# Kernel tuning notes

Hardware: AMD Instinct MI355X
Metric: run time of the kernel (lower is better)

Reference implementation:

```python
import jax, jax.numpy as jnp
import numpy as np

EMBED_DIM = 1024
NUM_HEADS = 16
HEAD_DIM = EMBED_DIM // NUM_HEADS
SCALE = EMBED_DIM ** (-0.5)  # NOTE: module scales by embed_dim**-0.5, not head_dim**-0.5


def setup_inputs() -> dict:
    key = jax.random.key(0)
    ks = jax.random.split(key, 10)
    B, N = 2, 2048
    q = jax.random.normal(ks[0], (B, N, EMBED_DIM), dtype=jnp.float32)
    kv = jax.random.normal(ks[1], (B, N, EMBED_DIM), dtype=jnp.float32)
    mask = jax.random.randint(ks[2], (B, N), 0, 2, dtype=jnp.int64)
    s = 0.02
    Wq = jax.random.normal(ks[3], (EMBED_DIM, EMBED_DIM), dtype=jnp.float32) * s
    bq = jax.random.normal(ks[4], (EMBED_DIM,), dtype=jnp.float32) * s
    Wkv = jax.random.normal(ks[5], (EMBED_DIM, 2 * EMBED_DIM), dtype=jnp.float32) * s
    bkv = jax.random.normal(ks[6], (2 * EMBED_DIM,), dtype=jnp.float32) * s
    Wo = jax.random.normal(ks[7], (EMBED_DIM, EMBED_DIM), dtype=jnp.float32) * s
    bo = jax.random.normal(ks[8], (EMBED_DIM,), dtype=jnp.float32) * s
    return {"q": q, "kv": kv, "mask": mask, "Wq": Wq, "bq": bq,
            "Wkv": Wkv, "bkv": bkv, "Wo": Wo, "bo": bo}


def _softmax_plus_one(x):
    # softmax with +1 in the denominator; max clipped at 0, no grad through max
    m = jax.lax.stop_gradient(jnp.maximum(jnp.max(x, axis=-1, keepdims=True), 0.0))
    unnorm = jnp.exp(x - m)
    denom = jnp.sum(unnorm, axis=-1, keepdims=True) + jnp.exp(-m)
    return unnorm / denom


def _split_heads(x):
    b, n, _ = x.shape
    return x.reshape(b, n, NUM_HEADS, HEAD_DIM).transpose(0, 2, 1, 3)  # b h n d


def reference(q, kv, mask, Wq, bq, Wkv, bkv, Wo, bo):
    xq = q @ Wq + bq
    xkv = kv @ Wkv + bkv
    xk, xv = jnp.split(xkv, 2, axis=-1)
    xq, xk, xv = _split_heads(xq), _split_heads(xk), _split_heads(xv)
    logits = jnp.einsum('bhnd,bhmd->bhnm', xq * SCALE, xk)
    # prepare_mask: log of 0/1 mask broadcast over (head, query) dims
    logmask = jnp.log(mask.astype(logits.dtype))[:, None, None, :]
    logits = logits + logmask
    # attn_dropout = 0.0 -> no-op
    scores = _softmax_plus_one(logits)  # add_one_to_softmax=True
    attn = jnp.einsum('bhnm,bhmd->bhnd', scores, xv)
    b, h, n, d = attn.shape
    out = attn.transpose(0, 2, 1, 3).reshape(b, n, h * d)
    return out @ Wo + bo
```

## Files before the change

### kernel.cpp

```cpp
#include <hip/hip_runtime.h>
#include <hip/hip_bf16.h>

static constexpr int CB = 2, CN = 2048, CE = 1024, CH = 16, CD = 64;
static constexpr int CM = CB * CN;
#define SCALE_Q (1.4426950408889634f / 32.0f)

typedef __attribute__((ext_vector_type(8))) short short8;
typedef __attribute__((ext_vector_type(4))) float f32x4;
typedef __attribute__((ext_vector_type(16))) float f32x16;
typedef __attribute__((ext_vector_type(4))) float f4;
typedef __attribute__((ext_vector_type(4))) unsigned short u16x4;

#define MFMA16(a, b, c) __builtin_amdgcn_mfma_f32_16x16x32_bf16((a), (b), (c), 0, 0, 0)
#define MFMA32(a, b, c) __builtin_amdgcn_mfma_f32_32x32x16_bf16((a), (b), (c), 0, 0, 0)

static __device__ __forceinline__ unsigned short f2bf(float f) {
  union { __hip_bfloat16 h; unsigned short u; } cv;
  cv.h = __float2bfloat16(f);
  return cv.u;
}
static __device__ __forceinline__ unsigned int pk2bf(float lo, float hi) {
  return (unsigned int)f2bf(lo) | ((unsigned int)f2bf(hi) << 16);
}

typedef unsigned int u32;
static __device__ __forceinline__ void gload16(const void* g, void* l) {
  __builtin_amdgcn_global_load_lds(
      (const __attribute__((address_space(1))) u32*)g,
      (__attribute__((address_space(3))) u32*)l, 16, 0, 0);
}

__global__ __launch_bounds__(256) void prep(
    const float* __restrict__ Wq, const float* __restrict__ Wkv,
    const float* __restrict__ Wo, unsigned short* __restrict__ WqT,
    unsigned short* __restrict__ WkvT, unsigned short* __restrict__ WoT,
    const int* __restrict__ mask, int* __restrict__ cidx, int* __restrict__ cnt) {
  __shared__ float tile[32][33];
  __shared__ int tsum[256];
  const int bid = blockIdx.x;
  const int t = threadIdx.x;
  if (bid < 4096) {
    const float* in; unsigned short* out; int C, tb;
    if (bid < 1024)      { in = Wq;  out = WqT;  C = 1024; tb = bid; }
    else if (bid < 3072) { in = Wkv; out = WkvT; C = 2048; tb = bid - 1024; }
    else                 { in = Wo;  out = WoT;  C = 1024; tb = bid - 3072; }
    const int R = 1024;
    int tc = C >> 5;
    int bc = tb % tc, br = tb / tc;
    int c = t & 31, r0 = t >> 5;
#pragma unroll
    for (int i = 0; i < 4; ++i) {
      int r = r0 + i * 8;
      tile[r][c] = in[(size_t)(br * 32 + r) * C + bc * 32 + c];
    }
    __syncthreads();
#pragma unroll
    for (int i = 0; i < 4; ++i) {
      int r = r0 + i * 8;
      out[(size_t)(bc * 32 + r) * R + br * 32 + c] = f2bf(tile[c][r]);
    }
  } else {
    const int b = bid - 4096;
    int m[8], s = 0;
#pragma unroll
    for (int i = 0; i < 8; ++i) {
      m[i] = mask[b * CN + t * 8 + i] != 0;
      s += m[i];
    }
    tsum[t] = s;
    __syncthreads();
    if (t == 0) {
      int acc = 0;
      for (int i = 0; i < 256; ++i) { int v = tsum[i]; tsum[i] = acc; acc += v; }
      cnt[b] = acc;
    }
    __syncthreads();
    int pos = tsum[t];
#pragma unroll
    for (int i = 0; i < 8; ++i)
      if (m[i]) cidx[b * CN + pos++] = t * 8 + i;
  }
}

template <bool AF32, bool OUT_BF16, bool VSPLIT, bool GATHER>
static __device__ __forceinline__ void gemm_body(
    char* lds, int bm, int bn,
    const void* __restrict__ Ap, const unsigned short* __restrict__ Bt,
    const float* __restrict__ bias, void* __restrict__ C0,
    unsigned short* __restrict__ C1, int N, int K, float outscale,
    const int* __restrict__ cidx, const int* __restrict__ cnt) {
  constexpr int ASTR = AF32 ? 40 : 32;
  unsigned short* As = (unsigned short*)lds;
  unsigned short* Bs = (unsigned short*)(lds + 2 * 64 * ASTR * 2);
  const int m0 = bm << 6, n0 = bn << 7;

  if constexpr (GATHER) {
    const int bb = m0 >> 11;
    const int ru = min((cnt[bb] + 63) & ~63, CN);
    if ((m0 & 2047) >= ru) return;
  }

  const int t = threadIdx.x;
  const int lane = t & 63, w = t >> 6;
  const int wr = w >> 1, wc = w & 1;
  const int fr = lane & 15, fg = lane >> 4;

  const int ach = t & 3;
  size_t arow;
  {
    int gr = m0 + (t >> 2);
    if constexpr (GATHER) {
      int bb = gr >> 11, r = gr & 2047;
      int cb_ = cnt[bb];
      int cr = r < cb_ ? r : (cb_ > 0 ? cb_ - 1 : 0);
      gr = bb * CN + cidx[bb * CN + cr];
    }
    arow = (size_t)gr * K;
  }

  f32x4 acc[2][4];
#pragma unroll
  for (int i = 0; i < 2; ++i)
#pragma unroll
    for (int j = 0; j < 4; ++j) acc[i][j] = (f32x4){0.f, 0.f, 0.f, 0.f};

  f4 a0, a1;
  auto ALOAD = [&](int k0) {
    const float* src = (const float*)Ap + arow + k0 + ach * 8;
    a0 = *(const f4*)src;
    a1 = *(const f4*)(src + 4);
  };
  auto AWRITE = [&](int bi) {
    short8 av;
#pragma unroll
    for (int j = 0; j < 4; ++j) av[j] = (short)f2bf(a0[j]);
#pragma unroll
    for (int j = 0; j < 4; ++j) av[4 + j] = (short)f2bf(a1[j]);
    *(short8*)&As[bi * 64 * ASTR + (t >> 2) * ASTR + ach * 8] = av;
  };
  auto BSTAGE = [&](int bi, int k0) {
#pragma unroll
    for (int i = 0; i < 2; ++i) {
      int idx = t + i * 256, row = idx >> 2, ch = idx & 3;
      gload16(Bt + (size_t)(n0 + row) * K + k0 + ch * 8, &Bs[bi * 128 * 32 + idx * 8]);
    }
    if constexpr (!AF32)
      gload16((const unsigned short*)Ap + arow + k0 + ach * 8, &As[bi * 64 * 32 + t * 8]);
  };

  if constexpr (AF32) { ALOAD(0); AWRITE(0); }
  BSTAGE(0, 0);
  __syncthreads();

  const int nt = K >> 5;
  int buf = 0;
  for (int tt = 0; tt < nt; ++tt) {
    const bool np = tt < nt - 1;
    if (np) {
      if constexpr (AF32) ALOAD((tt + 1) << 5);
      BSTAGE(buf ^ 1, (tt + 1) << 5);
    }
    if (np) {
      if constexpr (AF32) asm volatile("s_waitcnt vmcnt(4)" ::: "memory");
      else                asm volatile("s_waitcnt vmcnt(3)" ::: "memory");
    } else {
      asm volatile("s_waitcnt vmcnt(0)" ::: "memory");
    }
    __builtin_amdgcn_s_barrier();
    __builtin_amdgcn_sched_barrier(0);

    short8 af[2], bfv[4];
#pragma unroll
    for (int mi = 0; mi < 2; ++mi)
      af[mi] = *(const short8*)&As[buf * 64 * ASTR + (wr * 32 + mi * 16 + fr) * ASTR + fg * 8];
#pragma unroll
    for (int ni = 0; ni < 4; ++ni)
      bfv[ni] = *(const short8*)&Bs[buf * 128 * 32 + (wc * 64 + ni * 16 + fr) * 32 + fg * 8];
#pragma unroll
    for (int mi = 0; mi < 2; ++mi)
#pragma unroll
      for (int ni = 0; ni < 4; ++ni) acc[mi][ni] = MFMA16(af[mi], bfv[ni], acc[mi][ni]);
    if (np) {
      if constexpr (AF32) AWRITE(buf ^ 1);
    }
    asm volatile("s_waitcnt lgkmcnt(0)" ::: "memory");
    __builtin_amdgcn_s_barrier();
    __builtin_amdgcn_sched_barrier(0);
    buf ^= 1;
  }

#pragma unroll
  for (int mi = 0; mi < 2; ++mi) {
    int row0 = m0 + wr * 32 + mi * 16 + fg * 4;
#pragma unroll
    for (int ni = 0; ni < 4; ++ni) {
      int col = n0 + wc * 64 + ni * 16 + fr;
      float bv = bias[col];
      if constexpr (VSPLIT) {
        if (col < CE) {
#pragma unroll
          for (int rr = 0; rr < 4; ++rr)
            ((unsigned short*)C0)[(size_t)(row0 + rr) * CE + col] =
                f2bf((acc[mi][ni][rr] + bv) * outscale);
        } else {
          u16x4 pk;
#pragma unroll
          for (int rr = 0; rr < 4; ++rr) pk[rr] = f2bf((acc[mi][ni][rr] + bv) * outscale);
          int b = row0 / CN, n = row0 % CN;
          *(u16x4*)&C1[((size_t)b * CE + (col - CE)) * CN + n] = pk;
        }
      } else if constexpr (OUT_BF16) {
#pragma unroll
        for (int rr = 0; rr < 4; ++rr)
          ((unsigned short*)C0)[(size_t)(row0 + rr) * N + col] =
              f2bf((acc[mi][ni][rr] + bv) * outscale);
      } else {
#pragma unroll
        for (int rr = 0; rr < 4; ++rr)
          ((float*)C0)[(size_t)(row0 + rr) * N + col] = (acc[mi][ni][rr] + bv) * outscale;
      }
    }
  }
}

__global__ __launch_bounds__(256) void gemm_qkv(
    const float* __restrict__ q, const unsigned short* __restrict__ WqT,
    const float* __restrict__ bq, unsigned short* __restrict__ xq,
    const float* __restrict__ kv, const unsigned short* __restrict__ WkvT,
    const float* __restrict__ bkv, unsigned short* __restrict__ xk,
    unsigned short* __restrict__ xvT,
    const int* __restrict__ cidx, const int* __restrict__ cnt) {
  __shared__ char lds[2 * 64 * 40 * 2 + 2 * 128 * 32 * 2];
  const int bid = blockIdx.x;
  if (bid < 512) {
    gemm_body<true, true, false, false>(lds, bid >> 3, bid & 7, q, WqT, bq,
                                        xq, nullptr, CE, CE, SCALE_Q,
                                        nullptr, nullptr);
  } else {
    const int b2 = bid - 512;
    gemm_body<true, true, true, true>(lds, b2 >> 4, b2 & 15, kv, WkvT, bkv,
                                      xk, xvT, 2 * CE, CE, 1.0f, cidx, cnt);
  }
}

__global__ __launch_bounds__(256) void gemm_o(
    const unsigned short* __restrict__ attnA, const unsigned short* __restrict__ WoT,
    const float* __restrict__ bo, float* __restrict__ out) {
  __shared__ char lds[2 * 64 * 32 * 2 + 2 * 128 * 32 * 2];
  gemm_body<false, false, false, false>(lds, blockIdx.x >> 3, blockIdx.x & 7,
                                        attnA, WoT, bo, out, nullptr, CE, CE,
                                        1.0f, nullptr, nullptr);
}

__global__ __launch_bounds__(256, 2) void attn_fwd(
    unsigned short* __restrict__ xq,
    const unsigned short* __restrict__ xk,
    const unsigned short* __restrict__ xvT,
    const int* __restrict__ cnt) {
  __shared__ unsigned short Kt[64][72];
  __shared__ unsigned short Vt[64][72];
  __shared__ float dsh[4][32];

  const int bid = blockIdx.x;
  const int qblk = bid & 15;
  const int h = (bid >> 4) & 15;
  const int b = bid >> 8;
  const int t = threadIdx.x, lane = t & 63, w = t >> 6;
  const int l31 = lane & 31, h5 = lane >> 5;
  const int q0 = qblk * 128 + w * 32;

  const int cntb = cnt[b];
  const int nt = (cntb + 63) >> 6;

  short8 qf[4];
  {
    const unsigned short* qp =
        xq + ((size_t)(b * CN + q0 + l31)) * CE + h * CD + h5 * 8;
#pragma unroll
    for (int dk = 0; dk < 4; ++dk) qf[dk] = *(const short8*)(qp + dk * 16);
  }

  f32x16 o[2];
#pragma unroll
  for (int c = 0; c < 2; ++c)
#pragma unroll
    for (int i = 0; i < 16; ++i) o[c][i] = 0.f;
  float ls = 0.f;

  const int r0s = t >> 3, sl0 = t & 7;
  const int r1s = r0s + 32, sl1 = sl0;

  short8 rk[2], rv[2];
  if (nt > 0) {
    rk[0] = *(const short8*)(xk + ((size_t)(b * CN + r0s)) * CE + h * CD + sl0 * 8);
    rk[1] = *(const short8*)(xk + ((size_t)(b * CN + r1s)) * CE + h * CD + sl1 * 8);
    rv[0] = *(const short8*)(xvT + ((size_t)(b * CE + h * CD + r0s)) * CN + sl0 * 8);
    rv[1] = *(const short8*)(xvT + ((size_t)(b * CE + h * CD + r1s)) * CN + sl1 * 8);
  }

  for (int kt = 0; kt < nt; ++kt) {
    __syncthreads();
    *(short8*)&Kt[r0s][sl0 * 8] = rk[0];
    *(short8*)&Kt[r1s][sl1 * 8] = rk[1];
    *(short8*)&Vt[r0s][sl0 * 8] = rv[0];
    *(short8*)&Vt[r1s][sl1 * 8] = rv[1];
    __syncthreads();

    if (kt < nt - 1) {
      const int kn = (kt + 1) * 64;
      rk[0] = *(const short8*)(xk + ((size_t)(b * CN + kn + r0s)) * CE + h * CD + sl0 * 8);
      rk[1] = *(const short8*)(xk + ((size_t)(b * CN + kn + r1s)) * CE + h * CD + sl1 * 8);
      rv[0] = *(const short8*)(xvT + ((size_t)(b * CE + h * CD + r0s)) * CN + kn + sl0 * 8);
      rv[1] = *(const short8*)(xvT + ((size_t)(b * CE + h * CD + r1s)) * CN + kn + sl1 * 8);
    }

    short8 ka[2][4];
#pragma unroll
    for (int cb = 0; cb < 2; ++cb)
#pragma unroll
      for (int dk = 0; dk < 4; ++dk)
        ka[cb][dk] = *(const short8*)&Kt[cb * 32 + l31][(dk * 2 + h5) * 8];

    f32x16 s2[2];
#pragma unroll
    for (int cb = 0; cb < 2; ++cb) {
#pragma unroll
      for (int i = 0; i < 16; ++i) s2[cb][i] = 0.f;
#pragma unroll
      for (int dk = 0; dk < 4; ++dk)
        s2[cb] = MFMA32(ka[cb][dk], qf[dk], s2[cb]);
    }

    const bool tail = (kt == nt - 1) && (cntb & 63);
    unsigned int U[2][4][2];
#pragma unroll
    for (int cb = 0; cb < 2; ++cb) {
      float p[16];
#pragma unroll
      for (int i = 0; i < 16; ++i) {
        float sv = s2[cb][i];
        if (tail) {
          int cpos = kt * 64 + cb * 32 + (i & 3) + 8 * (i >> 2) + 4 * h5;
          sv = (cpos < cntb) ? sv : -30000.f;
        }
        p[i] = __builtin_amdgcn_exp2f(sv);
        ls += p[i];
      }
#pragma unroll
      for (int m = 0; m < 4; ++m) {
        U[cb][m][0] = pk2bf(p[4 * m], p[4 * m + 1]);
        U[cb][m][1] = pk2bf(p[4 * m + 2], p[4 * m + 3]);
      }
    }

    short8 vb[2][4];
#pragma unroll
    for (int nb = 0; nb < 2; ++nb)
#pragma unroll
      for (int kc = 0; kc < 4; ++kc)
        vb[nb][kc] = *(const short8*)&Vt[nb * 32 + l31][(kc * 2 + h5) * 8];

#pragma unroll
    for (int kc = 0; kc < 4; ++kc) {
      const int cb = kc >> 1, k2 = (kc & 1) * 2;
      unsigned int su0 = h5 ? U[cb][k2 + 1][0] : U[cb][k2][0];
      unsigned int su1 = h5 ? U[cb][k2 + 1][1] : U[cb][k2][1];
      unsigned int st0 = h5 ? U[cb][k2][0] : U[cb][k2 + 1][0];
      unsigned int st1 = h5 ? U[cb][k2][1] : U[cb][k2 + 1][1];
      unsigned int x0 = (unsigned int)__shfl_xor((int)st0, 32);
      unsigned int x1 = (unsigned int)__shfl_xor((int)st1, 32);
      union { unsigned int u[4]; short8 v; } pa;
      pa.u[0] = h5 ? x0 : su0;
      pa.u[1] = h5 ? x1 : su1;
      pa.u[2] = h5 ? su0 : x0;
      pa.u[3] = h5 ? su1 : x1;
#pragma unroll
      for (int nb = 0; nb < 2; ++nb)
        o[nb] = MFMA32(pa.v, vb[nb][kc], o[nb]);
    }
  }

  {
    float tot = ls + __shfl_xor(ls, 32);
    if (h5 == 0) dsh[w][l31] = 1.0f / (tot + 1.0f);
  }
  __syncthreads();
#pragma unroll
  for (int m = 0; m < 4; ++m) {
    f4 dn4 = *(const f4*)&dsh[w][m * 8 + h5 * 4];
#pragma unroll
    for (int rr = 0; rr < 4; ++rr) {
      int q = m * 8 + h5 * 4 + rr;
      size_t row = (size_t)(b * CN + q0 + q);
#pragma unroll
      for (int nb = 0; nb < 2; ++nb) {
        float val = o[nb][m * 4 + rr] * dn4[rr];
        xq[row * CE + h * CD + nb * 32 + l31] = f2bf(val);
      }
    }
  }
}

extern "C" void kernel_launch(void* const* d_in, const int* in_sizes, int n_in,
                              void* d_out, int out_size, void* d_ws, size_t ws_size,
                              hipStream_t stream) {
  const float* q    = (const float*)d_in[0];
  const float* kv   = (const float*)d_in[1];
  const int*   mask = (const int*)d_in[2];
  const float* Wq   = (const float*)d_in[3];
  const float* bq   = (const float*)d_in[4];
  const float* Wkv  = (const float*)d_in[5];
  const float* bkv  = (const float*)d_in[6];
  const float* Wo   = (const float*)d_in[7];
  const float* bo   = (const float*)d_in[8];
  (void)in_sizes; (void)n_in; (void)out_size; (void)ws_size;

  char* ws = (char*)d_ws;
  unsigned short* WoT  = (unsigned short*)(ws);
  unsigned short* xq   = (unsigned short*)(ws + (2u  << 20));
  unsigned short* xk   = (unsigned short*)(ws + (10u << 20));
  unsigned short* xvT  = (unsigned short*)(ws + (18u << 20));
  unsigned short* WqT  = (unsigned short*)(ws + (26u << 20));
  unsigned short* WkvT = (unsigned short*)(ws + (28u << 20));
  int*            cidx = (int*)(ws + (32u << 20));
  int*            cnt  = (int*)(ws + (32u << 20) + 16384);

  prep<<<4098, 256, 0, stream>>>(Wq, Wkv, Wo, WqT, WkvT, WoT, mask, cidx, cnt);

  gemm_qkv<<<1536, 256, 0, stream>>>(q, WqT, bq, xq, kv, WkvT, bkv, xk, xvT, cidx, cnt);

  attn_fwd<<<CB * CH * 16, 256, 0, stream>>>(xq, xk, xvT, cnt);

  gemm_o<<<512, 256, 0, stream>>>(xq, WoT, bo, (float*)d_out);
}
```

Baseline: 104.8 us.

## Triple-buffer GEMM via direct fp32 LDS loads with XOR swizzle and XCD-aware block remap

Rewrites the shared GEMM body to use a three-stage LDS ring filled by global_load_lds for both operands. The fp32 A operand is now copied straight into LDS and converted to bf16 at fragment-read time instead of being converted in registers before the store. An XOR swizzle replaces the row padding to avoid bank conflicts, and the wait counts are adjusted for two tiles in flight. Block indices in the GEMM and attention kernels are also remapped so consecutive blocks spread across the XCDs, aiming for better L2 locality. The costs are more LDS per block, which can lower occupancy, and conversion work repeated on every fragment read.

After: 109.5 us. 1.04x slower.

```diff
diff --git a/kernel.cpp b/kernel.cpp
--- a/kernel.cpp
+++ b/kernel.cpp
@@ -29,6 +29,13 @@
       (const __attribute__((address_space(1))) u32*)g,
       (__attribute__((address_space(3))) u32*)l, 16, 0, 0);
 }
+
+#define WAITV(NSTR)                                              \
+  do {                                                           \
+    asm volatile("s_waitcnt vmcnt(" NSTR ")" ::: "memory");      \
+    __builtin_amdgcn_s_barrier();                                \
+    __builtin_amdgcn_sched_barrier(0);                           \
+  } while (0)
 
 __global__ __launch_bounds__(256) void prep(
     const float* __restrict__ Wq, const float* __restrict__ Wkv,
@@ -89,9 +96,10 @@
     const float* __restrict__ bias, void* __restrict__ C0,
     unsigned short* __restrict__ C1, int N, int K, float outscale,
     const int* __restrict__ cidx, const int* __restrict__ cnt) {
-  constexpr int ASTR = AF32 ? 40 : 32;
-  unsigned short* As = (unsigned short*)lds;
-  unsigned short* Bs = (unsigned short*)(lds + 2 * 64 * ASTR * 2);
+  constexpr int ABYTES = AF32 ? 8192 : 4096;
+  constexpr int BBYTES = 8192;
+  char* Abuf = lds;
+  char* Bbuf = lds + 3 * ABYTES;
   const int m0 = bm << 6, n0 = bn << 7;
 
   if constexpr (GATHER) {
@@ -105,18 +113,46 @@
   const int wr = w >> 1, wc = w & 1;
   const int fr = lane & 15, fg = lane >> 4;
 
-  const int ach = t & 3;
-  size_t arow;
-  {
-    int gr = m0 + (t >> 2);
+  auto garow = [&](int gr) -> size_t {
     if constexpr (GATHER) {
       int bb = gr >> 11, r = gr & 2047;
       int cb_ = cnt[bb];
       int cr = r < cb_ ? r : (cb_ > 0 ? cb_ - 1 : 0);
       gr = bb * CN + cidx[bb * CN + cr];
     }
-    arow = (size_t)gr * K;
-  }
+    return (size_t)gr * K;
+  };
+
+  int ssA;
+  size_t arow0, arow1 = 0;
+  if constexpr (AF32) {
+    int row = t >> 3;
+    ssA = (t & 7) ^ (row & 7);
+    arow0 = garow(m0 + row);
+    arow1 = garow(m0 + row + 32);
+  } else {
+    int row = t >> 2;
+    ssA = (t & 3) ^ (row & 3);
+    arow0 = garow(m0 + row);
+  }
+  const int brow = t >> 2;
+  const int ssB = (t & 3) ^ (brow & 3);
+
+  auto STAGE = [&](int bi, int tti) {
+    const int k0 = tti << 5;
+    if constexpr (AF32) {
+      const float* A = (const float*)Ap;
+      gload16(A + arow0 + k0 + ssA * 4, Abuf + bi * ABYTES + t * 16);
+      gload16(A + arow1 + k0 + ssA * 4, Abuf + bi * ABYTES + (t + 256) * 16);
+    } else {
+      const unsigned short* A = (const unsigned short*)Ap;
+      gload16(A + arow0 + k0 + ssA * 8, Abuf + bi * ABYTES + t * 16);
+    }
+    gload16(Bt + (size_t)(n0 + brow) * K + k0 + ssB * 8,
+            Bbuf + bi * BBYTES + t * 16);
+    gload16(Bt + (size_t)(n0 + brow + 64) * K + k0 + ssB * 8,
+            Bbuf + bi * BBYTES + (t + 256) * 16);
+  };
 
   f32x4 acc[2][4];
 #pragma unroll
@@ -124,69 +160,51 @@
 #pragma unroll
     for (int j = 0; j < 4; ++j) acc[i][j] = (f32x4){0.f, 0.f, 0.f, 0.f};
 
-  f4 a0, a1;
-  auto ALOAD = [&](int k0) {
-    const float* src = (const float*)Ap + arow + k0 + ach * 8;
-    a0 = *(const f4*)src;
-    a1 = *(const f4*)(src + 4);
-  };
-  auto AWRITE = [&](int bi) {
-    short8 av;
-#pragma unroll
-    for (int j = 0; j < 4; ++j) av[j] = (short)f2bf(a0[j]);
-#pragma unroll
-    for (int j = 0; j < 4; ++j) av[4 + j] = (short)f2bf(a1[j]);
-    *(short8*)&As[bi * 64 * ASTR + (t >> 2) * ASTR + ach * 8] = av;
-  };
-  auto BSTAGE = [&](int bi, int k0) {
-#pragma unroll
-    for (int i = 0; i < 2; ++i) {
-      int idx = t + i * 256, row = idx >> 2, ch = idx & 3;
-      gload16(Bt + (size_t)(n0 + row) * K + k0 + ch * 8, &Bs[bi * 128 * 32 + idx * 8]);
-    }
-    if constexpr (!AF32)
-      gload16((const unsigned short*)Ap + arow + k0 + ach * 8, &As[bi * 64 * 32 + t * 8]);
-  };
-
-  if constexpr (AF32) { ALOAD(0); AWRITE(0); }
-  BSTAGE(0, 0);
-  __syncthreads();
-
   const int nt = K >> 5;
+  STAGE(0, 0);
+  if (nt > 1) STAGE(1, 1);
+
   int buf = 0;
   for (int tt = 0; tt < nt; ++tt) {
-    const bool np = tt < nt - 1;
-    if (np) {
-      if constexpr (AF32) ALOAD((tt + 1) << 5);
-      BSTAGE(buf ^ 1, (tt + 1) << 5);
-    }
-    if (np) {
-      if constexpr (AF32) asm volatile("s_waitcnt vmcnt(4)" ::: "memory");
-      else                asm volatile("s_waitcnt vmcnt(3)" ::: "memory");
-    } else {
-      asm volatile("s_waitcnt vmcnt(0)" ::: "memory");
-    }
-    __builtin_amdgcn_s_barrier();
-    __builtin_amdgcn_sched_barrier(0);
+    if (tt + 2 < nt) STAGE((tt + 2) % 3, tt + 2);
+    if (tt < nt - 2)       { if constexpr (AF32) WAITV("8"); else WAITV("6"); }
+    else if (tt == nt - 2) { if constexpr (AF32) WAITV("4"); else WAITV("3"); }
+    else                   WAITV("0");
 
     short8 af[2], bfv[4];
 #pragma unroll
+    for (int mi = 0; mi < 2; ++mi) {
+      const int r = wr * 32 + mi * 16 + fr;
+      if constexpr (AF32) {
+        const char* base = Abuf + buf * ABYTES + r * 128;
+        f4 lo = *(const f4*)(base + (((fg * 2) ^ (r & 7)) * 16));
+        f4 hi = *(const f4*)(base + (((fg * 2 + 1) ^ (r & 7)) * 16));
+        union { unsigned int u[4]; short8 v; } cv;
+        cv.u[0] = pk2bf(lo[0], lo[1]);
+        cv.u[1] = pk2bf(lo[2], lo[3]);
+        cv.u[2] = pk2bf(hi[0], hi[1]);
+        cv.u[3] = pk2bf(hi[2], hi[3]);
+        af[mi] = cv.v;
+      } else {
+        af[mi] = *(const short8*)(Abuf + buf * ABYTES + r * 64 +
+                                  ((fg ^ (r & 3)) * 16));
+      }
+    }
+#pragma unroll
+    for (int ni = 0; ni < 4; ++ni) {
+      const int r = wc * 64 + ni * 16 + fr;
+      bfv[ni] = *(const short8*)(Bbuf + buf * BBYTES + r * 64 +
+                                 ((fg ^ (r & 3)) * 16));
+    }
+#pragma unroll
     for (int mi = 0; mi < 2; ++mi)
-      af[mi] = *(const short8*)&As[buf * 64 * ASTR + (wr * 32 + mi * 16 + fr) * ASTR + fg * 8];
-#pragma unroll
-    for (int ni = 0; ni < 4; ++ni)
-      bfv[ni] = *(const short8*)&Bs[buf * 128 * 32 + (wc * 64 + ni * 16 + fr) * 32 + fg * 8];
-#pragma unroll
-    for (int mi = 0; mi < 2; ++mi)
 #pragma unroll
       for (int ni = 0; ni < 4; ++ni) acc[mi][ni] = MFMA16(af[mi], bfv[ni], acc[mi][ni]);
-    if (np) {
-      if constexpr (AF32) AWRITE(buf ^ 1);
-    }
+
     asm volatile("s_waitcnt lgkmcnt(0)" ::: "memory");
     __builtin_amdgcn_s_barrier();
     __builtin_amdgcn_sched_barrier(0);
-    buf ^= 1;
+    buf = (buf == 2) ? 0 : buf + 1;
   }
 
 #pragma unroll
@@ -230,8 +248,9 @@
     const float* __restrict__ bkv, unsigned short* __restrict__ xk,
     unsigned short* __restrict__ xvT,
     const int* __restrict__ cidx, const int* __restrict__ cnt) {
-  __shared__ char lds[2 * 64 * 40 * 2 + 2 * 128 * 32 * 2];
-  const int bid = blockIdx.x;
+  __shared__ char lds[3 * 8192 + 3 * 8192];
+  const int raw = blockIdx.x;
+  const int bid = (raw & 7) * 192 + (raw >> 3);
   if (bid < 512) {
     gemm_body<true, true, false, false>(lds, bid >> 3, bid & 7, q, WqT, bq,
                                         xq, nullptr, CE, CE, SCALE_Q,
@@ -246,8 +265,10 @@
 __global__ __launch_bounds__(256) void gemm_o(
     const unsigned short* __restrict__ attnA, const unsigned short* __restrict__ WoT,
     const float* __restrict__ bo, float* __restrict__ out) {
-  __shared__ char lds[2 * 64 * 32 * 2 + 2 * 128 * 32 * 2];
-  gemm_body<false, false, false, false>(lds, blockIdx.x >> 3, blockIdx.x & 7,
+  __shared__ char lds[3 * 4096 + 3 * 8192];
+  const int raw = blockIdx.x;
+  const int bid = (raw & 7) * 64 + (raw >> 3);
+  gemm_body<false, false, false, false>(lds, bid >> 3, bid & 7,
                                         attnA, WoT, bo, out, nullptr, CE, CE,
                                         1.0f, nullptr, nullptr);
 }
@@ -261,7 +282,8 @@
   __shared__ unsigned short Vt[64][72];
   __shared__ float dsh[4][32];
 
-  const int bid = blockIdx.x;
+  const int raw = blockIdx.x;
+  const int bid = (raw & 7) * 64 + (raw >> 3);
   const int qblk = bid & 15;
   const int h = (bid >> 4) & 15;
   const int b = bid >> 8;
```

## Triple-buffer GEMM LDS stages with two-tile-ahead prefetch

Applied to the files above, without the earlier changes.

Converts the shared GEMM body from double to triple buffering in LDS. Global loads for A (fp32 registers) and B (direct-to-LDS) are issued two K-tiles ahead, with ping-pong register sets for the fp32 A tile and a 2x-unrolled loop. This aims to hide global memory latency behind more MFMA work. In exchange it uses more LDS per block, which may reduce occupancy, and it needs more vmcnt bookkeeping.

After: 106.9 us. About the same (+1.9%).

```diff
diff --git a/kernel.cpp b/kernel.cpp
--- a/kernel.cpp
+++ b/kernel.cpp
@@ -29,6 +29,20 @@
       (const __attribute__((address_space(1))) u32*)g,
       (__attribute__((address_space(3))) u32*)l, 16, 0, 0);
 }
+
+#define SYNC_V(NSTR)                                             \
+  do {                                                           \
+    asm volatile("s_waitcnt vmcnt(" NSTR ")" ::: "memory");      \
+    __builtin_amdgcn_s_barrier();                                \
+    __builtin_amdgcn_sched_barrier(0);                           \
+  } while (0)
+#define SYNC_L()                                                 \
+  do {                                                           \
+    asm volatile("s_waitcnt lgkmcnt(0)" ::: "memory");           \
+    __builtin_amdgcn_s_barrier();                                \
+    __builtin_amdgcn_sched_barrier(0);                           \
+  } while (0)
+#define FENCE() __builtin_amdgcn_sched_barrier(0)
 
 __global__ __launch_bounds__(256) void prep(
     const float* __restrict__ Wq, const float* __restrict__ Wkv,
@@ -91,7 +105,7 @@
     const int* __restrict__ cidx, const int* __restrict__ cnt) {
   constexpr int ASTR = AF32 ? 40 : 32;
   unsigned short* As = (unsigned short*)lds;
-  unsigned short* Bs = (unsigned short*)(lds + 2 * 64 * ASTR * 2);
+  unsigned short* Bs = (unsigned short*)(lds + 3 * 64 * ASTR * 2);
   const int m0 = bm << 6, n0 = bn << 7;
 
   if constexpr (GATHER) {
@@ -124,20 +138,6 @@
 #pragma unroll
     for (int j = 0; j < 4; ++j) acc[i][j] = (f32x4){0.f, 0.f, 0.f, 0.f};
 
-  f4 a0, a1;
-  auto ALOAD = [&](int k0) {
-    const float* src = (const float*)Ap + arow + k0 + ach * 8;
-    a0 = *(const f4*)src;
-    a1 = *(const f4*)(src + 4);
-  };
-  auto AWRITE = [&](int bi) {
-    short8 av;
-#pragma unroll
-    for (int j = 0; j < 4; ++j) av[j] = (short)f2bf(a0[j]);
-#pragma unroll
-    for (int j = 0; j < 4; ++j) av[4 + j] = (short)f2bf(a1[j]);
-    *(short8*)&As[bi * 64 * ASTR + (t >> 2) * ASTR + ach * 8] = av;
-  };
   auto BSTAGE = [&](int bi, int k0) {
 #pragma unroll
     for (int i = 0; i < 2; ++i) {
@@ -148,45 +148,80 @@
       gload16((const unsigned short*)Ap + arow + k0 + ach * 8, &As[bi * 64 * 32 + t * 8]);
   };
 
-  if constexpr (AF32) { ALOAD(0); AWRITE(0); }
+  const int nt = K >> 5;
+  f4 aA0, aA1, aB0, aB1;
+
+  if constexpr (AF32) {
+    const float* src = (const float*)Ap + arow + ach * 8;
+    aA0 = *(const f4*)src;
+    aA1 = *(const f4*)(src + 4);
+    short8 av;
+#pragma unroll
+    for (int j = 0; j < 4; ++j) av[j] = (short)f2bf(aA0[j]);
+#pragma unroll
+    for (int j = 0; j < 4; ++j) av[4 + j] = (short)f2bf(aA1[j]);
+    *(short8*)&As[(t >> 2) * ASTR + ach * 8] = av;
+  }
+  FENCE();
   BSTAGE(0, 0);
-  __syncthreads();
-
-  const int nt = K >> 5;
-  int buf = 0;
-  for (int tt = 0; tt < nt; ++tt) {
-    const bool np = tt < nt - 1;
-    if (np) {
-      if constexpr (AF32) ALOAD((tt + 1) << 5);
-      BSTAGE(buf ^ 1, (tt + 1) << 5);
-    }
-    if (np) {
-      if constexpr (AF32) asm volatile("s_waitcnt vmcnt(4)" ::: "memory");
-      else                asm volatile("s_waitcnt vmcnt(3)" ::: "memory");
+  FENCE();
+  if constexpr (AF32) {
+    const float* src = (const float*)Ap + arow + 32 + ach * 8;
+    aB0 = *(const f4*)src;
+    aB1 = *(const f4*)(src + 4);
+  }
+  FENCE();
+  BSTAGE(1, 32);
+  asm volatile("s_waitcnt lgkmcnt(0)" ::: "memory");
+
+  auto STEP = [&](int tt, f4& la0, f4& la1, f4& wa0, f4& wa1) {
+    const int cur = tt % 3;
+    const bool p2 = (tt + 2) < nt;
+    if (p2) {
+      if constexpr (AF32) {
+        const float* src = (const float*)Ap + arow + ((tt + 2) << 5) + ach * 8;
+        la0 = *(const f4*)src;
+        la1 = *(const f4*)(src + 4);
+      }
+      FENCE();
+      BSTAGE((tt + 2) % 3, (tt + 2) << 5);
+    }
+    if (p2) {
+      if constexpr (AF32) SYNC_V("8"); else SYNC_V("6");
+    } else if (tt + 1 < nt) {
+      if constexpr (AF32) SYNC_V("4"); else SYNC_V("3");
     } else {
-      asm volatile("s_waitcnt vmcnt(0)" ::: "memory");
-    }
-    __builtin_amdgcn_s_barrier();
-    __builtin_amdgcn_sched_barrier(0);
+      SYNC_V("0");
+    }
 
     short8 af[2], bfv[4];
 #pragma unroll
     for (int mi = 0; mi < 2; ++mi)
-      af[mi] = *(const short8*)&As[buf * 64 * ASTR + (wr * 32 + mi * 16 + fr) * ASTR + fg * 8];
+      af[mi] = *(const short8*)&As[cur * 64 * ASTR + (wr * 32 + mi * 16 + fr) * ASTR + fg * 8];
 #pragma unroll
     for (int ni = 0; ni < 4; ++ni)
-      bfv[ni] = *(const short8*)&Bs[buf * 128 * 32 + (wc * 64 + ni * 16 + fr) * 32 + fg * 8];
+      bfv[ni] = *(const short8*)&Bs[cur * 128 * 32 + (wc * 64 + ni * 16 + fr) * 32 + fg * 8];
 #pragma unroll
     for (int mi = 0; mi < 2; ++mi)
 #pragma unroll
       for (int ni = 0; ni < 4; ++ni) acc[mi][ni] = MFMA16(af[mi], bfv[ni], acc[mi][ni]);
-    if (np) {
-      if constexpr (AF32) AWRITE(buf ^ 1);
-    }
-    asm volatile("s_waitcnt lgkmcnt(0)" ::: "memory");
-    __builtin_amdgcn_s_barrier();
-    __builtin_amdgcn_sched_barrier(0);
-    buf ^= 1;
+
+    if (tt + 1 < nt) {
+      if constexpr (AF32) {
+        short8 av;
+#pragma unroll
+        for (int j = 0; j < 4; ++j) av[j] = (short)f2bf(wa0[j]);
+#pragma unroll
+        for (int j = 0; j < 4; ++j) av[4 + j] = (short)f2bf(wa1[j]);
+        *(short8*)&As[((tt + 1) % 3) * 64 * ASTR + (t >> 2) * ASTR + ach * 8] = av;
+      }
+    }
+    SYNC_L();
+  };
+
+  for (int t2 = 0; t2 < nt; t2 += 2) {
+    STEP(t2,     aA0, aA1, aB0, aB1);
+    STEP(t2 + 1, aB0, aB1, aA0, aA1);
   }
 
 #pragma unroll
@@ -230,7 +265,7 @@
     const float* __restrict__ bkv, unsigned short* __restrict__ xk,
     unsigned short* __restrict__ xvT,
     const int* __restrict__ cidx, const int* __restrict__ cnt) {
-  __shared__ char lds[2 * 64 * 40 * 2 + 2 * 128 * 32 * 2];
+  __shared__ char lds[3 * 64 * 40 * 2 + 3 * 128 * 32 * 2];
   const int bid = blockIdx.x;
   if (bid < 512) {
     gemm_body<true, true, false, false>(lds, bid >> 3, bid & 7, q, WqT, bq,
@@ -246,7 +281,7 @@
 __global__ __launch_bounds__(256) void gemm_o(
     const unsigned short* __restrict__ attnA, const unsigned short* __restrict__ WoT,
     const float* __restrict__ bo, float* __restrict__ out) {
-  __shared__ char lds[2 * 64 * 32 * 2 + 2 * 128 * 32 * 2];
+  __shared__ char lds[3 * 64 * 32 * 2 + 3 * 128 * 32 * 2];
   gemm_body<false, false, false, false>(lds, blockIdx.x >> 3, blockIdx.x & 7,
                                         attnA, WoT, bo, out, nullptr, CE, CE,
                                         1.0f, nullptr, nullptr);
```

## Double GEMM K-tile to 64 and XOR-swizzle LDS staging for B and bf16 A

Applied to the files above, without the earlier changes.

The projection GEMMs now process a 64-wide K slice per iteration instead of 32, halving the number of loop iterations and barriers. Direct-to-LDS loads of the bf16 B tiles (and the bf16 A tile in the output GEMM) use a 128-byte row with an XOR swizzle on 16-byte chunks to avoid LDS bank conflicts. The fp32 A path loads twice as many values per thread with a padded stride of 72. LDS use per block roughly doubles and more registers are live per thread, which may reduce occupancy.

Measured after the change: 100.5 us. 1.04x faster.

```diff
diff --git a/kernel.cpp b/kernel.cpp
--- a/kernel.cpp
+++ b/kernel.cpp
@@ -29,6 +29,19 @@
       (const __attribute__((address_space(1))) u32*)g,
       (__attribute__((address_space(3))) u32*)l, 16, 0, 0);
 }
+
+#define SYNC_V(NSTR)                                             \
+  do {                                                           \
+    asm volatile("s_waitcnt vmcnt(" NSTR ")" ::: "memory");      \
+    __builtin_amdgcn_s_barrier();                                \
+    __builtin_amdgcn_sched_barrier(0);                           \
+  } while (0)
+#define SYNC_L()                                                 \
+  do {                                                           \
+    asm volatile("s_waitcnt lgkmcnt(0)" ::: "memory");           \
+    __builtin_amdgcn_s_barrier();                                \
+    __builtin_amdgcn_sched_barrier(0);                           \
+  } while (0)
 
 __global__ __launch_bounds__(256) void prep(
     const float* __restrict__ Wq, const float* __restrict__ Wkv,
@@ -89,9 +102,9 @@
     const float* __restrict__ bias, void* __restrict__ C0,
     unsigned short* __restrict__ C1, int N, int K, float outscale,
     const int* __restrict__ cidx, const int* __restrict__ cnt) {
-  constexpr int ASTR = AF32 ? 40 : 32;
+  constexpr int ASTR = AF32 ? 72 : 64;
   unsigned short* As = (unsigned short*)lds;
-  unsigned short* Bs = (unsigned short*)(lds + 2 * 64 * ASTR * 2);
+  char* Bs = lds + 2 * 64 * ASTR * 2;
   const int m0 = bm << 6, n0 = bn << 7;
 
   if constexpr (GATHER) {
@@ -104,6 +117,8 @@
   const int lane = t & 63, w = t >> 6;
   const int wr = w >> 1, wc = w & 1;
   const int fr = lane & 15, fg = lane >> 4;
+
+  const int sw8 = (t & 7) ^ ((t >> 3) & 7);
 
   const int ach = t & 3;
   size_t arow;
@@ -124,68 +139,100 @@
 #pragma unroll
     for (int j = 0; j < 4; ++j) acc[i][j] = (f32x4){0.f, 0.f, 0.f, 0.f};
 
-  f4 a0, a1;
+  f4 a0, a1, a2, a3;
   auto ALOAD = [&](int k0) {
     const float* src = (const float*)Ap + arow + k0 + ach * 8;
     a0 = *(const f4*)src;
     a1 = *(const f4*)(src + 4);
+    a2 = *(const f4*)(src + 32);
+    a3 = *(const f4*)(src + 36);
   };
   auto AWRITE = [&](int bi) {
-    short8 av;
-#pragma unroll
-    for (int j = 0; j < 4; ++j) av[j] = (short)f2bf(a0[j]);
-#pragma unroll
-    for (int j = 0; j < 4; ++j) av[4 + j] = (short)f2bf(a1[j]);
-    *(short8*)&As[bi * 64 * ASTR + (t >> 2) * ASTR + ach * 8] = av;
+    short8 av0, av1;
+#pragma unroll
+    for (int j = 0; j < 4; ++j) {
+      av0[j] = (short)f2bf(a0[j]);
+      av0[4 + j] = (short)f2bf(a1[j]);
+      av1[j] = (short)f2bf(a2[j]);
+      av1[4 + j] = (short)f2bf(a3[j]);
+    }
+    unsigned short* dst = As + bi * 64 * ASTR + (t >> 2) * ASTR;
+    *(short8*)&dst[ach * 8] = av0;
+    *(short8*)&dst[32 + ach * 8] = av1;
   };
   auto BSTAGE = [&](int bi, int k0) {
 #pragma unroll
-    for (int i = 0; i < 2; ++i) {
-      int idx = t + i * 256, row = idx >> 2, ch = idx & 3;
-      gload16(Bt + (size_t)(n0 + row) * K + k0 + ch * 8, &Bs[bi * 128 * 32 + idx * 8]);
-    }
-    if constexpr (!AF32)
-      gload16((const unsigned short*)Ap + arow + k0 + ach * 8, &As[bi * 64 * 32 + t * 8]);
+    for (int i = 0; i < 4; ++i) {
+      int s = t + i * 256;
+      gload16(Bt + (size_t)(n0 + (s >> 3)) * K + k0 + sw8 * 8,
+              Bs + bi * 128 * 128 + s * 16);
+    }
+    if constexpr (!AF32) {
+#pragma unroll
+      for (int i = 0; i < 2; ++i) {
+        int s = t + i * 256;
+        gload16((const unsigned short*)Ap + (size_t)(m0 + (s >> 3)) * K + k0 + sw8 * 8,
+                (char*)As + bi * 64 * 128 + s * 16);
+      }
+    }
   };
 
   if constexpr (AF32) { ALOAD(0); AWRITE(0); }
   BSTAGE(0, 0);
   __syncthreads();
 
-  const int nt = K >> 5;
+  const int nt = K >> 6;
   int buf = 0;
   for (int tt = 0; tt < nt; ++tt) {
     const bool np = tt < nt - 1;
     if (np) {
-      if constexpr (AF32) ALOAD((tt + 1) << 5);
-      BSTAGE(buf ^ 1, (tt + 1) << 5);
+      if constexpr (AF32) ALOAD((tt + 1) << 6);
+      BSTAGE(buf ^ 1, (tt + 1) << 6);
     }
     if (np) {
-      if constexpr (AF32) asm volatile("s_waitcnt vmcnt(4)" ::: "memory");
-      else                asm volatile("s_waitcnt vmcnt(3)" ::: "memory");
+      if constexpr (AF32) asm volatile("s_waitcnt vmcnt(8)" ::: "memory");
+      else                asm volatile("s_waitcnt vmcnt(6)" ::: "memory");
     } else {
       asm volatile("s_waitcnt vmcnt(0)" ::: "memory");
     }
     __builtin_amdgcn_s_barrier();
     __builtin_amdgcn_sched_barrier(0);
 
-    short8 af[2], bfv[4];
-#pragma unroll
-    for (int mi = 0; mi < 2; ++mi)
-      af[mi] = *(const short8*)&As[buf * 64 * ASTR + (wr * 32 + mi * 16 + fr) * ASTR + fg * 8];
-#pragma unroll
-    for (int ni = 0; ni < 4; ++ni)
-      bfv[ni] = *(const short8*)&Bs[buf * 128 * 32 + (wc * 64 + ni * 16 + fr) * 32 + fg * 8];
-#pragma unroll
-    for (int mi = 0; mi < 2; ++mi)
-#pragma unroll
-      for (int ni = 0; ni < 4; ++ni) acc[mi][ni] = MFMA16(af[mi], bfv[ni], acc[mi][ni]);
+    short8 af[2][2], bfv[4][2];
+#pragma unroll
+    for (int mi = 0; mi < 2; ++mi) {
+      const int r = wr * 32 + mi * 16 + fr;
+#pragma unroll
+      for (int kk = 0; kk < 2; ++kk) {
+        if constexpr (AF32) {
+          af[mi][kk] = *(const short8*)&As[buf * 64 * ASTR + r * ASTR + kk * 32 + fg * 8];
+        } else {
+          const int sl = (kk * 4 + fg) ^ (r & 7);
+          af[mi][kk] = *(const short8*)((char*)As + buf * 64 * 128 + r * 128 + sl * 16);
+        }
+      }
+    }
+#pragma unroll
+    for (int ni = 0; ni < 4; ++ni) {
+      const int r = wc * 64 + ni * 16 + fr;
+#pragma unroll
+      for (int kk = 0; kk < 2; ++kk) {
+        const int sl = (kk * 4 + fg) ^ (r & 7);
+        bfv[ni][kk] = *(const short8*)(Bs + buf * 128 * 128 + r * 128 + sl * 16);
+      }
+    }
+#pragma unroll
+    for (int kk = 0; kk < 2; ++kk)
+#pragma unroll
+      for (int mi = 0; mi < 2; ++mi)
+#pragma unroll
+        for (int ni = 0; ni < 4; ++ni)
+          acc[mi][ni] = MFMA16(af[mi][kk], bfv[ni][kk], acc[mi][ni]);
+
     if (np) {
       if constexpr (AF32) AWRITE(buf ^ 1);
     }
-    asm volatile("s_waitcnt lgkmcnt(0)" ::: "memory");
-    __builtin_amdgcn_s_barrier();
-    __builtin_amdgcn_sched_barrier(0);
+    SYNC_L();
     buf ^= 1;
   }
 
@@ -230,7 +277,7 @@
     const float* __restrict__ bkv, unsigned short* __restrict__ xk,
     unsigned short* __restrict__ xvT,
     const int* __restrict__ cidx, const int* __restrict__ cnt) {
-  __shared__ char lds[2 * 64 * 40 * 2 + 2 * 128 * 32 * 2];
+  __shared__ char lds[2 * 64 * 72 * 2 + 2 * 128 * 128];
   const int bid = blockIdx.x;
   if (bid < 512) {
     gemm_body<true, true, false, false>(lds, bid >> 3, bid & 7, q, WqT, bq,
@@ -246,7 +293,7 @@
 __global__ __launch_bounds__(256) void gemm_o(
     const unsigned short* __restrict__ attnA, const unsigned short* __restrict__ WoT,
     const float* __restrict__ bo, float* __restrict__ out) {
-  __shared__ char lds[2 * 64 * 32 * 2 + 2 * 128 * 32 * 2];
+  __shared__ char lds[2 * 64 * 128 + 2 * 128 * 128];
   gemm_body<false, false, false, false>(lds, blockIdx.x >> 3, blockIdx.x & 7,
                                         attnA, WoT, bo, out, nullptr, CE, CE,
                                         1.0f, nullptr, nullptr);
```
